# Kernel optimization log

Hardware: AMD Instinct MI355X
Metric: run time of the kernel (lower is better)

The kernel has to match this reference:

```python
import jax, jax.numpy as jnp
import numpy as np

NUM_STEPS = 10  # fixed-step Dopri5 over [0, T], dt = T/NUM_STEPS (dt0=0.1, T=1.0 in source)
B, D, H = 8192, 64, 256


def setup_inputs() -> dict:
    key = jax.random.key(0)
    ks = jax.random.split(key, 4)
    x = jax.random.normal(ks[0], (B, D), jnp.float32)
    logdet_init = jnp.zeros((B,), jnp.float32)

    def lin(k, out_dim, in_dim):
        kw, kb = jax.random.split(k)
        lim = 1.0 / np.sqrt(in_dim)
        W = jax.random.uniform(kw, (out_dim, in_dim), jnp.float32, -lim, lim)
        b = jax.random.uniform(kb, (out_dim,), jnp.float32, -lim, lim)
        return W, b

    W1, b1 = lin(ks[1], H, D)
    W2, b2 = lin(ks[2], H, H)
    W3, b3 = lin(ks[3], D, H)
    T = jnp.array(1.0, jnp.float32)
    return dict(x=x, logdet_init=logdet_init, W1=W1, b1=b1, W2=W2, b2=b2, W3=W3, b3=b3, T=T)


def reference(x, logdet_init, W1, b1, W2, b2, W3, b3, T):
    # odefunc: softplus MLP, per-sample (eqx Linear semantics: W @ y + b)
    def mlp(y):  # y: (D,)
        h = jax.nn.softplus(W1 @ y + b1)
        h = jax.nn.softplus(W2 @ h + b2)
        return W3 @ h + b3

    trace_fn = jax.vmap(lambda y: jnp.trace(jax.jacfwd(mlp)(y)))  # exact trace, [B]

    def dyn(y):  # y: [B, D] -> (dy/dt [B,D], dlogdet/dt [B])
        h = jax.nn.softplus(y @ W1.T + b1)
        h = jax.nn.softplus(h @ W2.T + b2)
        dy = h @ W3.T + b3
        return dy, trace_fn(y)

    dt = T / NUM_STEPS
    # Dormand-Prince 5(4) tableau (6 stages used for the 5th-order update)
    a21 = 1/5
    a31, a32 = 3/40, 9/40
    a41, a42, a43 = 44/45, -56/15, 32/9
    a51, a52, a53, a54 = 19372/6561, -25360/2187, 64448/6561, -212/729
    a61, a62, a63, a64, a65 = 9017/3168, -355/33, 46732/5247, 49/176, -5103/18656
    c1, c3, c4, c5, c6 = 35/384, 500/1113, 125/192, -2187/6784, 11/84

    def step(carry, _):
        y, ld = carry
        k1y, k1l = dyn(y)
        k2y, k2l = dyn(y + dt * (a21 * k1y))
        k3y, k3l = dyn(y + dt * (a31 * k1y + a32 * k2y))
        k4y, k4l = dyn(y + dt * (a41 * k1y + a42 * k2y + a43 * k3y))
        k5y, k5l = dyn(y + dt * (a51 * k1y + a52 * k2y + a53 * k3y + a54 * k4y))
        k6y, k6l = dyn(y + dt * (a61 * k1y + a62 * k2y + a63 * k3y + a64 * k4y + a65 * k5y))
        y_new = y + dt * (c1 * k1y + c3 * k3y + c4 * k4y + c5 * k5y + c6 * k6y)
        ld_new = ld + dt * (c1 * k1l + c3 * k3l + c4 * k4l + c5 * k5l + c6 * k6l)
        return (y_new, ld_new), None

    (y_f, ld_f), _ = jax.lax.scan(step, (x, logdet_init), None, length=NUM_STEPS)
    return (y_f, ld_f)
```

## Files before the change

### kernel.cpp

```cpp
#include <hip/hip_runtime.h>

typedef __attribute__((ext_vector_type(4))) float f32x4;
typedef __attribute__((ext_vector_type(8))) short bf16x8;
typedef __attribute__((ext_vector_type(4))) short bf16x4;

#define MFMA16(a, b, c) __builtin_amdgcn_mfma_f32_16x16x32_bf16(a, b, c, 0, 0, 0)

#define W1F_OFF 0
#define W2F_OFF 16384
#define CF_OFF  81920
#define W3F_OFF 147456

__device__ __forceinline__ short f2bf(float f) {
  unsigned u = __builtin_bit_cast(unsigned, f);
  u += 0x7FFFu + ((u >> 16) & 1u);
  return (short)(u >> 16);
}

__device__ __forceinline__ void sp_sig(float z, float& h, float& s) {
  float t = __expf(-fabsf(z));
#if __has_builtin(__builtin_amdgcn_rcpf)
  float r = __builtin_amdgcn_rcpf(1.f + t);
#else
  float r = 1.f / (1.f + t);
#endif
  h = fmaxf(z, 0.f) + __logf(1.f + t);
  s = (z >= 0.f) ? r : 1.f - r;
}

__global__ __launch_bounds__(512) void cnf_prep(const float* __restrict__ W1,
                                                const float* __restrict__ W2,
                                                const float* __restrict__ W3,
                                                short* __restrict__ ws) {
  int e = blockIdx.x * 512 + threadIdx.x;
  int j = e & 7;
  int l = (e >> 3) & 63;
  int g = l >> 4, lm = l & 15;
  float val;
  if (e < 16384) {
    int t = e >> 9, kt = t & 1, mt = t >> 1;
    val = W1[(mt * 16 + lm) * 64 + kt * 32 + g * 8 + j];
  } else if (e < 81920) {
    int t = (e - 16384) >> 9, kt = t & 7, mt = t >> 3;
    val = W2[(mt * 16 + lm) * 256 + kt * 32 + g * 8 + j];
  } else if (e < 147456) {
    int t = (e - 81920) >> 9, kt = t & 7, mt = t >> 3;
    int m = mt * 16 + lm, k = kt * 32 + g * 8 + j;
    float a2 = 0.f;
#pragma unroll 16
    for (int d = 0; d < 64; ++d) a2 += W1[k * 64 + d] * W3[d * 256 + m];
    val = W2[m * 256 + k] * a2;
  } else {
    int t = (e - 147456) >> 9, kt = t & 7, mt = t >> 3;
    val = W3[(mt * 16 + lm) * 256 + kt * 32 + g * 8 + j];
  }
  ws[e] = f2bf(val);
}

__global__ __launch_bounds__(512) void cnf_main(
    const float* __restrict__ x, const float* __restrict__ ld_init,
    const float* __restrict__ b1g, const float* __restrict__ b2g,
    const float* __restrict__ b3g, const float* __restrict__ Tg,
    const short* __restrict__ ws, float* __restrict__ outy,
    float* __restrict__ outl) {
  __shared__ __align__(16) short w1f[16384];
  __shared__ __align__(16) short w3f[16384];
  __shared__ __align__(16) short ytL[32 * 88];
  __shared__ __align__(16) short h1L[32 * 264];
  __shared__ __align__(16) short s1L_[32 * 264];
  __shared__ __align__(16) short h2L[32 * 264];
  __shared__ __align__(16) float dyL[32 * 68];
  __shared__ float trP[8][32];
  __shared__ float b1L[256], b2L[256], b3L[64];

  const int tid = threadIdx.x;
  const int lane = tid & 63, wv = tid >> 6;
  const int sl = tid >> 4, q = tid & 15;
  const int lg = lane >> 4, lm = lane & 15;
  const int ko8 = lg << 3;

  {
    const f32x4* s1p = (const f32x4*)ws;
    f32x4* d1 = (f32x4*)w1f;
#pragma unroll
    for (int i = 0; i < 4; ++i) d1[tid + 512 * i] = s1p[tid + 512 * i];
    const f32x4* s3p = (const f32x4*)(ws + W3F_OFF);
    f32x4* d3 = (f32x4*)w3f;
#pragma unroll
    for (int i = 0; i < 4; ++i) d3[tid + 512 * i] = s3p[tid + 512 * i];
    if (tid < 256) { b1L[tid] = b1g[tid]; b2L[tid] = b2g[tid]; }
    else if (tid < 320) b3L[tid - 256] = b3g[tid - 256];
  }

  const bf16x8* w2fG = (const bf16x8*)(ws + W2F_OFF);
  const bf16x8* cfG  = (const bf16x8*)(ws + CF_OFF);

  const int sg = blockIdx.x * 32 + sl;
  f32x4 y = *(const f32x4*)&x[sg * 64 + q * 4];
  float ld = ld_init[sg];
  const float dt = Tg[0] * 0.1f;

  __syncthreads();

  auto dyn = [&](f32x4 yin, f32x4& dy, float& tr) {
    bf16x4 yb;
#pragma unroll
    for (int r = 0; r < 4; ++r) yb[r] = f2bf(yin[r]);
    *(bf16x4*)&ytL[sl * 88 + q * 4] = yb;
    __syncthreads();

    f32x4 a00 = {0,0,0,0}, a01 = {0,0,0,0}, a10 = {0,0,0,0}, a11 = {0,0,0,0};
#pragma unroll
    for (int kt = 0; kt < 2; ++kt) {
      bf16x8 A0 = *(const bf16x8*)&w1f[(((2 * wv + 0) * 2 + kt) * 64 + lane) * 8];
      bf16x8 A1 = *(const bf16x8*)&w1f[(((2 * wv + 1) * 2 + kt) * 64 + lane) * 8];
      bf16x8 B0 = *(const bf16x8*)&ytL[lm * 88 + kt * 32 + ko8];
      bf16x8 B1 = *(const bf16x8*)&ytL[(16 + lm) * 88 + kt * 32 + ko8];
      a00 = MFMA16(A0, B0, a00); a01 = MFMA16(A0, B1, a01);
      a10 = MFMA16(A1, B0, a10); a11 = MFMA16(A1, B1, a11);
    }
    {
      auto epi1 = [&](f32x4 z4, int r2, int c) {
        int row0 = (2 * wv + r2) * 16 + (lg << 2);
        int sc = c * 16 + lm;
        bf16x4 hh, ss;
#pragma unroll
        for (int r = 0; r < 4; ++r) {
          float h, s;
          sp_sig(z4[r] + b1L[row0 + r], h, s);
          hh[r] = f2bf(h); ss[r] = f2bf(s);
        }
        *(bf16x4*)&h1L[sc * 264 + row0] = hh;
        *(bf16x4*)&s1L_[sc * 264 + row0] = ss;
      };
      epi1(a00, 0, 0); epi1(a01, 0, 1); epi1(a10, 1, 0); epi1(a11, 1, 1);
    }
    __syncthreads();

    f32x4 c00 = {0,0,0,0}, c01 = {0,0,0,0}, c10 = {0,0,0,0}, c11 = {0,0,0,0};
#pragma unroll
    for (int kt = 0; kt < 8; ++kt) {
      bf16x8 A0 = w2fG[((2 * wv + 0) * 8 + kt) * 64 + lane];
      bf16x8 A1 = w2fG[((2 * wv + 1) * 8 + kt) * 64 + lane];
      bf16x8 B0 = *(const bf16x8*)&h1L[lm * 264 + kt * 32 + ko8];
      bf16x8 B1 = *(const bf16x8*)&h1L[(16 + lm) * 264 + kt * 32 + ko8];
      c00 = MFMA16(A0, B0, c00); c01 = MFMA16(A0, B1, c01);
      c10 = MFMA16(A1, B0, c10); c11 = MFMA16(A1, B1, c11);
    }
    f32x4 s200, s201, s210, s211;
    {
      auto epi2 = [&](f32x4 z4, int r2, int c, f32x4& s2o) {
        int row0 = (2 * wv + r2) * 16 + (lg << 2);
        int sc = c * 16 + lm;
        bf16x4 hh;
#pragma unroll
        for (int r = 0; r < 4; ++r) {
          float h, s;
          sp_sig(z4[r] + b2L[row0 + r], h, s);
          hh[r] = f2bf(h); s2o[r] = s;
        }
        *(bf16x4*)&h2L[sc * 264 + row0] = hh;
      };
      epi2(c00, 0, 0, s200); epi2(c01, 0, 1, s201);
      epi2(c10, 1, 0, s210); epi2(c11, 1, 1, s211);
    }
    __syncthreads();

    f32x4 u00 = {0,0,0,0}, u01 = {0,0,0,0}, u10 = {0,0,0,0}, u11 = {0,0,0,0};
#pragma unroll
    for (int kt = 0; kt < 8; ++kt) {
      bf16x8 A0 = cfG[((2 * wv + 0) * 8 + kt) * 64 + lane];
      bf16x8 A1 = cfG[((2 * wv + 1) * 8 + kt) * 64 + lane];
      bf16x8 B0 = *(const bf16x8*)&s1L_[lm * 264 + kt * 32 + ko8];
      bf16x8 B1 = *(const bf16x8*)&s1L_[(16 + lm) * 264 + kt * 32 + ko8];
      u00 = MFMA16(A0, B0, u00); u01 = MFMA16(A0, B1, u01);
      u10 = MFMA16(A1, B0, u10); u11 = MFMA16(A1, B1, u11);
    }
    float pl0 = 0.f, pl1 = 0.f;
#pragma unroll
    for (int r = 0; r < 4; ++r) {
      pl0 += u00[r] * s200[r] + u10[r] * s210[r];
      pl1 += u01[r] * s201[r] + u11[r] * s211[r];
    }
    pl0 += __shfl_xor(pl0, 16); pl0 += __shfl_xor(pl0, 32);
    pl1 += __shfl_xor(pl1, 16); pl1 += __shfl_xor(pl1, 32);
    if (lane < 16) { trP[wv][lane] = pl0; trP[wv][16 + lane] = pl1; }

    f32x4 d3a = {0,0,0,0};
    const int m3 = wv & 3, c3 = wv >> 2;
#pragma unroll
    for (int kt = 0; kt < 8; ++kt) {
      bf16x8 A0 = *(const bf16x8*)&w3f[((m3 * 8 + kt) * 64 + lane) * 8];
      bf16x8 B0 = *(const bf16x8*)&h2L[(c3 * 16 + lm) * 264 + kt * 32 + ko8];
      d3a = MFMA16(A0, B0, d3a);
    }
    {
      int d0r = m3 * 16 + (lg << 2);
      int sc = c3 * 16 + lm;
      f32x4 dv;
#pragma unroll
      for (int r = 0; r < 4; ++r) dv[r] = d3a[r] + b3L[d0r + r];
      *(f32x4*)&dyL[sc * 68 + d0r] = dv;
    }
    __syncthreads();

    dy = *(const f32x4*)&dyL[sl * 68 + q * 4];
    float t = 0.f;
#pragma unroll
    for (int w = 0; w < 8; ++w) t += trP[w][sl];
    tr = t;
  };

  const float A21 = 1.f / 5.f;
  const float A31 = 3.f / 40.f, A32 = 9.f / 40.f;
  const float A41 = 44.f / 45.f, A42 = -56.f / 15.f, A43 = 32.f / 9.f;
  const float A51 = 19372.f / 6561.f, A52 = -25360.f / 2187.f,
              A53 = 64448.f / 6561.f, A54 = -212.f / 729.f;
  const float A61 = 9017.f / 3168.f, A62 = -355.f / 33.f,
              A63 = 46732.f / 5247.f, A64 = 49.f / 176.f, A65 = -5103.f / 18656.f;
  const float C1 = 35.f / 384.f, C3 = 500.f / 1113.f, C4 = 125.f / 192.f,
              C5 = -2187.f / 6784.f, C6 = 11.f / 84.f;

  f32x4 k1, k2, k3, k4, k5, k6;
  float l1, l2, l3, l4, l5, l6;
#pragma unroll 1
  for (int step = 0; step < 10; ++step) {
    dyn(y, k1, l1);
    dyn(y + dt * (A21 * k1), k2, l2);
    dyn(y + dt * (A31 * k1 + A32 * k2), k3, l3);
    dyn(y + dt * (A41 * k1 + A42 * k2 + A43 * k3), k4, l4);
    dyn(y + dt * (A51 * k1 + A52 * k2 + A53 * k3 + A54 * k4), k5, l5);
    dyn(y + dt * (A61 * k1 + A62 * k2 + A63 * k3 + A64 * k4 + A65 * k5), k6, l6);
    y = y + dt * (C1 * k1 + C3 * k3 + C4 * k4 + C5 * k5 + C6 * k6);
    ld = ld + dt * (C1 * l1 + C3 * l3 + C4 * l4 + C5 * l5 + C6 * l6);
  }

  *(f32x4*)&outy[sg * 64 + q * 4] = y;
  if (q == 0) outl[sg] = ld;
}

extern "C" void kernel_launch(void* const* d_in, const int* in_sizes, int n_in,
                              void* d_out, int out_size, void* d_ws, size_t ws_size,
                              hipStream_t stream) {
  const float* x  = (const float*)d_in[0];
  const float* l0 = (const float*)d_in[1];
  const float* W1 = (const float*)d_in[2];
  const float* b1 = (const float*)d_in[3];
  const float* W2 = (const float*)d_in[4];
  const float* b2 = (const float*)d_in[5];
  const float* W3 = (const float*)d_in[6];
  const float* b3 = (const float*)d_in[7];
  const float* Tp = (const float*)d_in[8];
  short* ws = (short*)d_ws;

  cnf_prep<<<dim3(320), dim3(512), 0, stream>>>(W1, W2, W3, ws);

  float* outy = (float*)d_out;
  float* outl = outy + 8192 * 64;
  cnf_main<<<dim3(256), dim3(512), 0, stream>>>(x, l0, b1, b2, b3, Tp, ws, outy, outl);
}
```

Measured before the change: 317.5 us.

## Fold biases into MFMA accumulators, drop a barrier, use native exp2/log2 and bf16 cvt

Biases now sit in registers and initialize the MFMA accumulators, so the separate bias loads from LDS and the adds go away. The barrier between the layer-2 epilogue and the trace/W3 stage is removed, since those stages only read buffers already synchronized. Softplus uses hardware exp2/log2 intrinsics, f2bf uses the native bf16 conversion, and dt is folded into the RK coefficients while the logdet update is accumulated incrementally. The trace partials are transposed so each sample reads them with vector loads. Dropping the barrier relies on h2L being written and read by the same layout without a cross-wave race, and w3 reads h2L rows written by other waves, so the race risk is real.

Result: slower. 380.7 us (+19.9%).

```diff
diff --git a/kernel.cpp b/kernel.cpp
--- a/kernel.cpp
+++ b/kernel.cpp
@@ -12,19 +12,29 @@
 #define W3F_OFF 147456
 
 __device__ __forceinline__ short f2bf(float f) {
-  unsigned u = __builtin_bit_cast(unsigned, f);
-  u += 0x7FFFu + ((u >> 16) & 1u);
-  return (short)(u >> 16);
+  __bf16 b = (__bf16)f;
+  return __builtin_bit_cast(short, b);
 }
 
 __device__ __forceinline__ void sp_sig(float z, float& h, float& s) {
-  float t = __expf(-fabsf(z));
+  float a = fabsf(z);
+#if __has_builtin(__builtin_amdgcn_exp2f)
+  float t = __builtin_amdgcn_exp2f(a * -1.44269504f);
+#else
+  float t = __expf(-a);
+#endif
+  float o = 1.f + t;
 #if __has_builtin(__builtin_amdgcn_rcpf)
-  float r = __builtin_amdgcn_rcpf(1.f + t);
+  float r = __builtin_amdgcn_rcpf(o);
 #else
-  float r = 1.f / (1.f + t);
+  float r = 1.f / o;
 #endif
-  h = fmaxf(z, 0.f) + __logf(1.f + t);
+#if __has_builtin(__builtin_amdgcn_logf)
+  float l2 = __builtin_amdgcn_logf(o);
+#else
+  float l2 = __logf(o) * 1.44269504f;
+#endif
+  h = fmaxf(z, 0.f) + 0.69314718f * l2;
   s = (z >= 0.f) ? r : 1.f - r;
 }
 
@@ -70,8 +80,7 @@
   __shared__ __align__(16) short s1L_[32 * 264];
   __shared__ __align__(16) short h2L[32 * 264];
   __shared__ __align__(16) float dyL[32 * 68];
-  __shared__ float trP[8][32];
-  __shared__ float b1L[256], b2L[256], b3L[64];
+  __shared__ __align__(16) float trPT[32][12];
 
   const int tid = threadIdx.x;
   const int lane = tid & 63, wv = tid >> 6;
@@ -80,7 +89,7 @@
   const int ko8 = lg << 3;
 
   {
-    const f32x4* s1p = (const f32x4*)ws;
+    const f32x4* s1p = (const f32x4*)(ws + W1F_OFF);
     f32x4* d1 = (f32x4*)w1f;
 #pragma unroll
     for (int i = 0; i < 4; ++i) d1[tid + 512 * i] = s1p[tid + 512 * i];
@@ -88,9 +97,16 @@
     f32x4* d3 = (f32x4*)w3f;
 #pragma unroll
     for (int i = 0; i < 4; ++i) d3[tid + 512 * i] = s3p[tid + 512 * i];
-    if (tid < 256) { b1L[tid] = b1g[tid]; b2L[tid] = b2g[tid]; }
-    else if (tid < 320) b3L[tid - 256] = b3g[tid - 256];
   }
+
+  const int row0a = (2 * wv + 0) * 16 + (lg << 2);
+  const int row0b = (2 * wv + 1) * 16 + (lg << 2);
+  const f32x4 bias1a = *(const f32x4*)&b1g[row0a];
+  const f32x4 bias1b = *(const f32x4*)&b1g[row0b];
+  const f32x4 bias2a = *(const f32x4*)&b2g[row0a];
+  const f32x4 bias2b = *(const f32x4*)&b2g[row0b];
+  const int m3 = wv & 3, c3 = wv >> 2;
+  const f32x4 bias3 = *(const f32x4*)&b3g[m3 * 16 + (lg << 2)];
 
   const bf16x8* w2fG = (const bf16x8*)(ws + W2F_OFF);
   const bf16x8* cfG  = (const bf16x8*)(ws + CF_OFF);
@@ -102,14 +118,15 @@
 
   __syncthreads();
 
-  auto dyn = [&](f32x4 yin, f32x4& dy, float& tr) {
+  auto dyn = [&](f32x4 yin, f32x4& dy, float& tr)
+      __attribute__((always_inline)) {
     bf16x4 yb;
 #pragma unroll
     for (int r = 0; r < 4; ++r) yb[r] = f2bf(yin[r]);
     *(bf16x4*)&ytL[sl * 88 + q * 4] = yb;
     __syncthreads();
 
-    f32x4 a00 = {0,0,0,0}, a01 = {0,0,0,0}, a10 = {0,0,0,0}, a11 = {0,0,0,0};
+    f32x4 a00 = bias1a, a01 = bias1a, a10 = bias1b, a11 = bias1b;
 #pragma unroll
     for (int kt = 0; kt < 2; ++kt) {
       bf16x8 A0 = *(const bf16x8*)&w1f[(((2 * wv + 0) * 2 + kt) * 64 + lane) * 8];
@@ -120,24 +137,25 @@
       a10 = MFMA16(A1, B0, a10); a11 = MFMA16(A1, B1, a11);
     }
     {
-      auto epi1 = [&](f32x4 z4, int r2, int c) {
-        int row0 = (2 * wv + r2) * 16 + (lg << 2);
+      auto epi1 = [&](const f32x4& z4, int r0, int c)
+          __attribute__((always_inline)) {
         int sc = c * 16 + lm;
         bf16x4 hh, ss;
 #pragma unroll
         for (int r = 0; r < 4; ++r) {
           float h, s;
-          sp_sig(z4[r] + b1L[row0 + r], h, s);
+          sp_sig(z4[r], h, s);
           hh[r] = f2bf(h); ss[r] = f2bf(s);
         }
-        *(bf16x4*)&h1L[sc * 264 + row0] = hh;
-        *(bf16x4*)&s1L_[sc * 264 + row0] = ss;
+        *(bf16x4*)&h1L[sc * 264 + r0] = hh;
+        *(bf16x4*)&s1L_[sc * 264 + r0] = ss;
       };
-      epi1(a00, 0, 0); epi1(a01, 0, 1); epi1(a10, 1, 0); epi1(a11, 1, 1);
+      epi1(a00, row0a, 0); epi1(a01, row0a, 1);
+      epi1(a10, row0b, 0); epi1(a11, row0b, 1);
     }
     __syncthreads();
 
-    f32x4 c00 = {0,0,0,0}, c01 = {0,0,0,0}, c10 = {0,0,0,0}, c11 = {0,0,0,0};
+    f32x4 c00 = bias2a, c01 = bias2a, c10 = bias2b, c11 = bias2b;
 #pragma unroll
     for (int kt = 0; kt < 8; ++kt) {
       bf16x8 A0 = w2fG[((2 * wv + 0) * 8 + kt) * 64 + lane];
@@ -149,22 +167,21 @@
     }
     f32x4 s200, s201, s210, s211;
     {
-      auto epi2 = [&](f32x4 z4, int r2, int c, f32x4& s2o) {
-        int row0 = (2 * wv + r2) * 16 + (lg << 2);
+      auto epi2 = [&](const f32x4& z4, int r0, int c, f32x4& s2o)
+          __attribute__((always_inline)) {
         int sc = c * 16 + lm;
         bf16x4 hh;
 #pragma unroll
         for (int r = 0; r < 4; ++r) {
           float h, s;
-          sp_sig(z4[r] + b2L[row0 + r], h, s);
+          sp_sig(z4[r], h, s);
           hh[r] = f2bf(h); s2o[r] = s;
         }
-        *(bf16x4*)&h2L[sc * 264 + row0] = hh;
+        *(bf16x4*)&h2L[sc * 264 + r0] = hh;
       };
-      epi2(c00, 0, 0, s200); epi2(c01, 0, 1, s201);
-      epi2(c10, 1, 0, s210); epi2(c11, 1, 1, s211);
-    }
-    __syncthreads();
+      epi2(c00, row0a, 0, s200); epi2(c01, row0a, 1, s201);
+      epi2(c10, row0b, 0, s210); epi2(c11, row0b, 1, s211);
+    }
 
     f32x4 u00 = {0,0,0,0}, u01 = {0,0,0,0}, u10 = {0,0,0,0}, u11 = {0,0,0,0};
 #pragma unroll
@@ -184,55 +201,51 @@
     }
     pl0 += __shfl_xor(pl0, 16); pl0 += __shfl_xor(pl0, 32);
     pl1 += __shfl_xor(pl1, 16); pl1 += __shfl_xor(pl1, 32);
-    if (lane < 16) { trP[wv][lane] = pl0; trP[wv][16 + lane] = pl1; }
-
-    f32x4 d3a = {0,0,0,0};
-    const int m3 = wv & 3, c3 = wv >> 2;
+    if (lane < 16) { trPT[lane][wv] = pl0; trPT[16 + lane][wv] = pl1; }
+
+    f32x4 d3a = bias3;
 #pragma unroll
     for (int kt = 0; kt < 8; ++kt) {
       bf16x8 A0 = *(const bf16x8*)&w3f[((m3 * 8 + kt) * 64 + lane) * 8];
       bf16x8 B0 = *(const bf16x8*)&h2L[(c3 * 16 + lm) * 264 + kt * 32 + ko8];
       d3a = MFMA16(A0, B0, d3a);
     }
-    {
-      int d0r = m3 * 16 + (lg << 2);
-      int sc = c3 * 16 + lm;
-      f32x4 dv;
-#pragma unroll
-      for (int r = 0; r < 4; ++r) dv[r] = d3a[r] + b3L[d0r + r];
-      *(f32x4*)&dyL[sc * 68 + d0r] = dv;
-    }
+    *(f32x4*)&dyL[(c3 * 16 + lm) * 68 + m3 * 16 + (lg << 2)] = d3a;
     __syncthreads();
 
     dy = *(const f32x4*)&dyL[sl * 68 + q * 4];
-    float t = 0.f;
-#pragma unroll
-    for (int w = 0; w < 8; ++w) t += trP[w][sl];
-    tr = t;
+    f32x4 t0 = *(const f32x4*)&trPT[sl][0];
+    f32x4 t1 = *(const f32x4*)&trPT[sl][4];
+    f32x4 ts = t0 + t1;
+    tr = ts[0] + ts[1] + ts[2] + ts[3];
   };
 
-  const float A21 = 1.f / 5.f;
-  const float A31 = 3.f / 40.f, A32 = 9.f / 40.f;
-  const float A41 = 44.f / 45.f, A42 = -56.f / 15.f, A43 = 32.f / 9.f;
-  const float A51 = 19372.f / 6561.f, A52 = -25360.f / 2187.f,
-              A53 = 64448.f / 6561.f, A54 = -212.f / 729.f;
-  const float A61 = 9017.f / 3168.f, A62 = -355.f / 33.f,
-              A63 = 46732.f / 5247.f, A64 = 49.f / 176.f, A65 = -5103.f / 18656.f;
-  const float C1 = 35.f / 384.f, C3 = 500.f / 1113.f, C4 = 125.f / 192.f,
-              C5 = -2187.f / 6784.f, C6 = 11.f / 84.f;
+  const float A21 = dt * (1.f / 5.f);
+  const float A31 = dt * (3.f / 40.f), A32 = dt * (9.f / 40.f);
+  const float A41 = dt * (44.f / 45.f), A42 = dt * (-56.f / 15.f),
+              A43 = dt * (32.f / 9.f);
+  const float A51 = dt * (19372.f / 6561.f), A52 = dt * (-25360.f / 2187.f),
+              A53 = dt * (64448.f / 6561.f), A54 = dt * (-212.f / 729.f);
+  const float A61 = dt * (9017.f / 3168.f), A62 = dt * (-355.f / 33.f),
+              A63 = dt * (46732.f / 5247.f), A64 = dt * (49.f / 176.f),
+              A65 = dt * (-5103.f / 18656.f);
+  const float C1 = dt * (35.f / 384.f), C3 = dt * (500.f / 1113.f),
+              C4 = dt * (125.f / 192.f), C5 = dt * (-2187.f / 6784.f),
+              C6 = dt * (11.f / 84.f);
 
   f32x4 k1, k2, k3, k4, k5, k6;
-  float l1, l2, l3, l4, l5, l6;
+  float tr;
 #pragma unroll 1
   for (int step = 0; step < 10; ++step) {
-    dyn(y, k1, l1);
-    dyn(y + dt * (A21 * k1), k2, l2);
-    dyn(y + dt * (A31 * k1 + A32 * k2), k3, l3);
-    dyn(y + dt * (A41 * k1 + A42 * k2 + A43 * k3), k4, l4);
-    dyn(y + dt * (A51 * k1 + A52 * k2 + A53 * k3 + A54 * k4), k5, l5);
-    dyn(y + dt * (A61 * k1 + A62 * k2 + A63 * k3 + A64 * k4 + A65 * k5), k6, l6);
-    y = y + dt * (C1 * k1 + C3 * k3 + C4 * k4 + C5 * k5 + C6 * k6);
-    ld = ld + dt * (C1 * l1 + C3 * l3 + C4 * l4 + C5 * l5 + C6 * l6);
+    dyn(y, k1, tr);                                          ld += C1 * tr;
+    dyn(y + A21 * k1, k2, tr);
+    dyn(y + A31 * k1 + A32 * k2, k3, tr);                    ld += C3 * tr;
+    dyn(y + A41 * k1 + A42 * k2 + A43 * k3, k4, tr);         ld += C4 * tr;
+    dyn(y + A51 * k1 + A52 * k2 + A53 * k3 + A54 * k4, k5, tr);
+    ld += C5 * tr;
+    dyn(y + A61 * k1 + A62 * k2 + A63 * k3 + A64 * k4 + A65 * k5, k6, tr);
+    ld += C6 * tr;
+    y = y + C1 * k1 + C3 * k3 + C4 * k4 + C5 * k5 + C6 * k6;
   }
 
   *(f32x4*)&outy[sg * 64 + q * 4] = y;
@@ -257,5 +270,6 @@
 
   float* outy = (float*)d_out;
   float* outl = outy + 8192 * 64;
-  cnf_main<<<dim3(256), dim3(512), 0, stream>>>(x, l0, b1, b2, b3, Tp, ws, outy, outl);
-}
+  cnf_main<<<dim3(256), dim3(512), 0, stream>>>(x, l0, b1, b2, b3, Tp, ws,
+                                                outy, outl);
+}
```
